# Optimization experiments

Measured on AMD Instinct MI355X. Metric: run time of the kernel, lower is better.

Reference implementation:

```python
import jax, jax.numpy as jnp
import numpy as np

N, E, L = 50000, 300000, 4
DN, DE, H, DO = 11, 3, 128, 2


def _ln(x, g, b, eps=1e-5):
    m = jnp.mean(x, axis=-1, keepdims=True)
    v = jnp.mean((x - m) ** 2, axis=-1, keepdims=True)
    return (x - m) * jax.lax.rsqrt(v + eps) * g + b


def _mlp(x, w1, b1, w2, b2, g, be):
    # Linear -> ReLU -> Linear -> LayerNorm (matches torch Sequential)
    h = jax.nn.relu(x @ w1 + b1)
    return _ln(h @ w2 + b2, g, be)


def setup_inputs() -> dict:
    key = jax.random.key(0)
    ks = iter(jax.random.split(key, 64))
    def nrm(shape, s=1.0):
        return jax.random.normal(next(ks), shape, jnp.float32) * s
    w = 0.02  # weight init scale
    inp = {
        'x': nrm((N, DN)),
        'edge_index': jax.random.randint(next(ks), (2, E), 0, N, jnp.int32),
        'edge_attr': nrm((E, DE)),
        'mean_vec_x': nrm((DN,)),
        'std_vec_x': jnp.ones((DN,), jnp.float32),
        'mean_vec_edge': nrm((DE,)),
        'std_vec_edge': jnp.ones((DE,), jnp.float32),
        # node encoder
        'ne_w1': nrm((DN, H), w), 'ne_b1': jnp.zeros((H,), jnp.float32),
        'ne_w2': nrm((H, H), w), 'ne_b2': jnp.zeros((H,), jnp.float32),
        'ne_g': jnp.ones((H,), jnp.float32), 'ne_be': jnp.zeros((H,), jnp.float32),
        # edge encoder
        'ee_w1': nrm((DE, H), w), 'ee_b1': jnp.zeros((H,), jnp.float32),
        'ee_w2': nrm((H, H), w), 'ee_b2': jnp.zeros((H,), jnp.float32),
        'ee_g': jnp.ones((H,), jnp.float32), 'ee_be': jnp.zeros((H,), jnp.float32),
        # processor edge MLPs (stacked over L layers): Linear(3H->H), Linear(H->H), LN
        'pe_w1': nrm((L, 3 * H, H), w), 'pe_b1': jnp.zeros((L, H), jnp.float32),
        'pe_w2': nrm((L, H, H), w), 'pe_b2': jnp.zeros((L, H), jnp.float32),
        'pe_g': jnp.ones((L, H), jnp.float32), 'pe_be': jnp.zeros((L, H), jnp.float32),
        # processor node MLPs: Linear(2H->H), Linear(H->H), LN
        'pn_w1': nrm((L, 2 * H, H), w), 'pn_b1': jnp.zeros((L, H), jnp.float32),
        'pn_w2': nrm((L, H, H), w), 'pn_b2': jnp.zeros((L, H), jnp.float32),
        'pn_g': jnp.ones((L, H), jnp.float32), 'pn_be': jnp.zeros((L, H), jnp.float32),
        # decoder: Linear(H->H) ReLU Linear(H->DO)
        'de_w1': nrm((H, H), w), 'de_b1': jnp.zeros((H,), jnp.float32),
        'de_w2': nrm((H, DO), w), 'de_b2': jnp.zeros((DO,), jnp.float32),
    }
    return inp


def reference(x, edge_index, edge_attr, mean_vec_x, std_vec_x, mean_vec_edge, std_vec_edge,
              ne_w1, ne_b1, ne_w2, ne_b2, ne_g, ne_be,
              ee_w1, ee_b1, ee_w2, ee_b2, ee_g, ee_be,
              pe_w1, pe_b1, pe_w2, pe_b2, pe_g, pe_be,
              pn_w1, pn_b1, pn_w2, pn_b2, pn_g, pn_be,
              de_w1, de_b1, de_w2, de_b2):
    x = (x - mean_vec_x) / std_vec_x
    e = (edge_attr - mean_vec_edge) / std_vec_edge
    x = _mlp(x, ne_w1, ne_b1, ne_w2, ne_b2, ne_g, ne_be)   # [N, H]
    e = _mlp(e, ee_w1, ee_b1, ee_w2, ee_b2, ee_g, ee_be)   # [E, H]
    row, col = edge_index[0], edge_index[1]
    for i in range(L):
        # edge update: gather endpoints, concat with edge feature, residual
        msg_in = jnp.concatenate([x[row], x[col], e], axis=-1)  # [E, 3H]
        e = e + _mlp(msg_in, pe_w1[i], pe_b1[i], pe_w2[i], pe_b2[i], pe_g[i], pe_be[i])
        # aggregate messages (= updated edge_attr) at target nodes (col), sum-aggr
        agg = jax.ops.segment_sum(e, col, num_segments=N)       # [N, H]
        node_in = jnp.concatenate([x, agg], axis=-1)             # [N, 2H]
        x = x + _mlp(node_in, pn_w1[i], pn_b1[i], pn_w2[i], pn_b2[i], pn_g[i], pn_be[i])
    return jax.nn.relu(x @ de_w1 + de_b1) @ de_w2 + de_b2       # [N, DO]
```

## Files before the change

### kernel.cpp

```cpp
#include <hip/hip_runtime.h>
#include <hip/hip_bf16.h>


#define NN 50000
#define EE 300000

typedef unsigned int u32;
typedef unsigned short u16;
typedef __attribute__((ext_vector_type(8))) short bf16x8;
typedef __attribute__((ext_vector_type(4))) float f32x4;

__device__ __forceinline__ float bf2f(u16 v){ return __uint_as_float(((u32)v) << 16); }
__device__ __forceinline__ u16 f2bf(float f){
  u32 u = __float_as_uint(f);
  return (u16)((u + 0x7fffu + ((u >> 16) & 1u)) >> 16);
}
#define MFMA __builtin_amdgcn_mfma_f32_16x16x32_bf16

struct CD { const void* src; float* dst; int n; };
struct IngestArgs { CD d[34]; };

__global__ __launch_bounds__(256)
void ingest_kernel(IngestArgs a, const u32* __restrict__ probe) {
  const bool isbf = (probe[0] == 0x3F803F80u);
  const CD c = a.d[blockIdx.y];
  for (int i = blockIdx.x*256 + threadIdx.x; i < c.n; i += gridDim.x*256) {
    c.dst[i] = isbf ? bf2f(((const u16*)c.src)[i]) : ((const float*)c.src)[i];
  }
}

struct PackDesc { const float* src; u16* dst; int K; int Ksrc; };
struct PackArgs { PackDesc d[20]; };

__global__ __launch_bounds__(256)
void pack_b_kernel(PackArgs pa) {
  const PackDesc p = pa.d[blockIdx.y];
  const int total = (p.K >> 5) * 512;
  for (int idx = blockIdx.x*256 + threadIdx.x; idx < total; idx += gridDim.x*256) {
    const int lane = idx & 63;
    const int tile = idx >> 6;
    const int nt = tile & 7, kt = tile >> 3;
    const int col = nt*16 + (lane & 15);
    const int k0  = kt*32 + (lane >> 4) * 8;
    u32 w4[4];
    #pragma unroll
    for (int jj = 0; jj < 4; ++jj) {
      const int ka = k0 + 2*jj, kb = k0 + 2*jj + 1;
      const u16 lo = (ka < p.Ksrc) ? f2bf(p.src[(size_t)ka * 128 + col]) : (u16)0;
      const u16 hi = (kb < p.Ksrc) ? f2bf(p.src[(size_t)kb * 128 + col]) : (u16)0;
      w4[jj] = (u32)lo | ((u32)hi << 16);
    }
    *(uint4*)(p.dst + (size_t)idx * 8) = make_uint4(w4[0], w4[1], w4[2], w4[3]);
  }
}

__global__ __launch_bounds__(256)
void zero_kernel(int4* __restrict__ p, int n4) {
  for (int i = blockIdx.x*256 + threadIdx.x; i < n4; i += gridDim.x*256)
    p[i] = make_int4(0, 0, 0, 0);
}

__global__ __launch_bounds__(256)
void hist_kernel(const int* __restrict__ ei, int* __restrict__ deg) {
  for (int i = blockIdx.x*256 + threadIdx.x; i < EE; i += gridDim.x*256)
    atomicAdd(&deg[ei[EE + i]], 1);
}

__global__ __launch_bounds__(1024)
void scan_kernel(const int* __restrict__ deg, int* __restrict__ start,
                 int* __restrict__ cursor) {
  __shared__ int sums[1024];
  const int t = threadIdx.x;
  const int base = t * 49;
  int s = 0;
  for (int j = 0; j < 49; ++j) { const int i = base + j; if (i < NN) s += deg[i]; }
  sums[t] = s; __syncthreads();
  for (int off = 1; off < 1024; off <<= 1) {
    int v = (t >= off) ? sums[t - off] : 0;
    __syncthreads();
    sums[t] += v;
    __syncthreads();
  }
  int ex = (t == 0) ? 0 : sums[t - 1];
  for (int j = 0; j < 49; ++j) {
    const int i = base + j;
    if (i < NN) { start[i] = ex; cursor[i] = ex; ex += deg[i]; }
  }
  if (t == 1023) start[NN] = ex;
}

__global__ __launch_bounds__(256)
void scatter_kernel(const int* __restrict__ ei, int* __restrict__ cursor,
                    int* __restrict__ perm, int* __restrict__ src_p,
                    int* __restrict__ dst_p) {
  for (int i = blockIdx.x*256 + threadIdx.x; i < EE; i += gridDim.x*256) {
    const int c = ei[EE + i];
    const int pos = atomicAdd(&cursor[c], 1);
    perm[pos]  = i;
    src_p[pos] = ei[i];
    dst_p[pos] = c;
  }
}

template<int KIN, int MODE>
__global__ __launch_bounds__(256)
void enc_mfma(const u16* __restrict__ w1pk, const float* __restrict__ b1,
              const u16* __restrict__ w2pk, const float* __restrict__ b2,
              const float* __restrict__ g,  const float* __restrict__ be,
              const float* __restrict__ raw, const float* __restrict__ mean,
              const float* __restrict__ stdv, const int* __restrict__ perm,
              float* __restrict__ x, u16* __restrict__ outb, int nrows)
{
  constexpr int STR = 296;
  __shared__ u16 As[64 * STR];
  const int lane  = threadIdx.x & 63;
  const int wv    = threadIdx.x >> 6;
  const int col_l = lane & 15;
  const int quad  = lane >> 4;
  const int m0    = wv * 16;
  const int r0    = blockIdx.x * 64;

  for (int t = lane; t < 256; t += 64)
    ((u32*)As)[(m0 + (t >> 4)) * 148 + (t & 15)] = 0u;
  for (int t = lane; t < 16 * KIN; t += 64) {
    const int r = t / KIN, k = t - r * KIN;
    int srow = min(r0 + m0 + r, nrows - 1);
    if constexpr (MODE == 1) srow = perm[srow];
    const float v = (raw[(size_t)srow * KIN + k] - mean[k]) / stdv[k];
    As[(m0 + r) * STR + k] = f2bf(v);
  }

  float b1v[8], b2v[8], gv[8], bev[8];
  #pragma unroll
  for (int nt = 0; nt < 8; ++nt) {
    b1v[nt] = b1[nt*16 + col_l]; b2v[nt] = b2[nt*16 + col_l];
    gv[nt]  = g [nt*16 + col_l]; bev[nt] = be[nt*16 + col_l];
  }

  const f32x4 zf = {0.f, 0.f, 0.f, 0.f};
  const bf16x8* bq1 = (const bf16x8*)w1pk;
  const bf16x8* bq2 = (const bf16x8*)w2pk;
  const u16* arow = As + (size_t)(m0 + col_l) * STR + quad * 8;

  f32x4 acc[8];
  #pragma unroll
  for (int nt = 0; nt < 8; ++nt) acc[nt] = zf;
  {
    const bf16x8 af = *(const bf16x8*)(arow);
    #pragma unroll
    for (int nt = 0; nt < 8; ++nt)
      acc[nt] = MFMA(af, bq1[nt*64 + lane], acc[nt], 0, 0, 0);
  }
  #pragma unroll
  for (int nt = 0; nt < 8; ++nt) {
    #pragma unroll
    for (int rg = 0; rg < 4; ++rg) {
      const float hv = fmaxf(acc[nt][rg] + b1v[nt], 0.f);
      As[(size_t)(m0 + quad*4 + rg) * STR + 32 + nt*16 + col_l] = f2bf(hv);
    }
  }
  f32x4 acc2[8];
  #pragma unroll
  for (int nt = 0; nt < 8; ++nt) acc2[nt] = zf;
  #pragma unroll
  for (int kt = 0; kt < 4; ++kt) {
    const bf16x8 af = *(const bf16x8*)(arow + 32 + kt * 32);
    #pragma unroll
    for (int nt = 0; nt < 8; ++nt)
      acc2[nt] = MFMA(af, bq2[(kt*8+nt)*64 + lane], acc2[nt], 0, 0, 0);
  }
  #pragma unroll
  for (int rg = 0; rg < 4; ++rg) {
    float v[8];
    float s1 = 0.f, s2 = 0.f;
    #pragma unroll
    for (int nt = 0; nt < 8; ++nt) {
      v[nt] = acc2[nt][rg] + b2v[nt];
      s1 += v[nt]; s2 += v[nt]*v[nt];
    }
    #pragma unroll
    for (int off = 1; off < 16; off <<= 1) {
      s1 += __shfl_xor(s1, off);
      s2 += __shfl_xor(s2, off);
    }
    const float mu   = s1 * (1.f/128.f);
    const float var  = s2 * (1.f/128.f) - mu*mu;
    const float rstd = rsqrtf(var + 1e-5f);
    const int rloc = m0 + quad*4 + rg;
    const int row  = r0 + rloc;
    #pragma unroll
    for (int nt = 0; nt < 8; ++nt) {
      const float y = (v[nt] - mu) * rstd * gv[nt] + bev[nt];
      As[(size_t)rloc * STR + 160 + nt*16 + col_l] = f2bf(y);
      if (MODE == 0 && row < nrows) x[(size_t)row*128 + nt*16 + col_l] = y;
    }
  }
  #pragma unroll
  for (int r = 0; r < 16; ++r) {
    const int row = r0 + m0 + r;
    if (row < nrows)
      ((u32*)(outb + (size_t)row * 128))[lane] =
          ((const u32*)(As + (size_t)(m0 + r) * STR + 160))[lane];
  }
}

__global__ __launch_bounds__(256, 1)
void edge_mfma(const u16* __restrict__ w1pk, const float* __restrict__ b1,
               const u16* __restrict__ w2pk, const float* __restrict__ b2,
               const float* __restrict__ g, const float* __restrict__ be,
               const u16* __restrict__ xb, u16* __restrict__ eb,
               const int* __restrict__ src_p, const int* __restrict__ dst_p)
{
  extern __shared__ u16 lds[];
  u16* lw1 = lds;
  u16* lh  = lds + 49152;

  const int lane = threadIdx.x & 63;
  const int wv   = threadIdx.x >> 6;
  const int m    = lane & 15;
  const int q    = lane >> 4;
  const int rbase = wv * 32;

  for (int i = threadIdx.x; i < 6144; i += 256)
    ((uint4*)lw1)[i] = ((const uint4*)w1pk)[i];

  bf16x8 w2r[32];
  #pragma unroll
  for (int f = 0; f < 32; ++f)
    w2r[f] = ((const bf16x8*)w2pk)[f*64 + lane];

  float b1v[8], b2v[8], gv[8], bev[8];
  #pragma unroll
  for (int nt = 0; nt < 8; ++nt) {
    b1v[nt] = b1[nt*16 + m]; b2v[nt] = b2[nt*16 + m];
    gv[nt]  = g [nt*16 + m]; bev[nt] = be[nt*16 + m];
  }
  __syncthreads();

  const int ntiles = (EE + 127) >> 7;
  bf16x8 A[2][12];

  auto loadA = [&](int t) {
    #pragma unroll
    for (int ms = 0; ms < 2; ++ms) {
      const int grow = min(t*128 + rbase + ms*16 + m, EE-1);
      const u16* p0 = xb + (size_t)src_p[grow] * 128 + q*8;
      const u16* p1 = xb + (size_t)dst_p[grow] * 128 + q*8;
      const u16* p2 = eb + (size_t)grow * 128 + q*8;
      #pragma unroll
      for (int kt = 0; kt < 4; ++kt) {
        A[ms][kt]   = *(const bf16x8*)(p0 + kt*32);
        A[ms][4+kt] = *(const bf16x8*)(p1 + kt*32);
        A[ms][8+kt] = *(const bf16x8*)(p2 + kt*32);
      }
    }
  };

  loadA(blockIdx.x);
  for (int t = blockIdx.x; t < ntiles; t += 256) {
    #pragma unroll
    for (int nt = 0; nt < 8; ++nt) {
      f32x4 c0 = {0.f,0.f,0.f,0.f}, c1 = {0.f,0.f,0.f,0.f};
      #pragma unroll
      for (int kt = 0; kt < 12; ++kt) {
        const bf16x8 bf = *(const bf16x8*)(lw1 + (size_t)(kt*8+nt)*512 + lane*8);
        c0 = MFMA(A[0][kt], bf, c0, 0, 0, 0);
        c1 = MFMA(A[1][kt], bf, c1, 0, 0, 0);
      }
      #pragma unroll
      for (int ms = 0; ms < 2; ++ms) {
        #pragma unroll
        for (int rg = 0; rg < 4; ++rg) {
          const float cc = (ms == 0) ? c0[rg] : c1[rg];
          const float hv = fmaxf(cc + b1v[nt], 0.f);
          const int row = rbase + ms*16 + q*4 + rg;
          const int col = nt*16 + m;
          lh[row*128 + ((((col>>3) ^ (row&7)))<<3) + (col&7)] = f2bf(hv);
        }
      }
    }
    const int tn = t + 256;
    if (tn < ntiles) loadA(tn);
    f32x4 acc2[2][8];
    #pragma unroll
    for (int ms = 0; ms < 2; ++ms)
      #pragma unroll
      for (int nt = 0; nt < 8; ++nt) acc2[ms][nt] = {0.f,0.f,0.f,0.f};
    #pragma unroll
    for (int kt2 = 0; kt2 < 4; ++kt2) {
      const int ra = rbase + m, rb = rbase + 16 + m;
      const bf16x8 h0 = *(const bf16x8*)(lh + ra*128 + (((kt2*4+q) ^ (ra&7))<<3));
      const bf16x8 h1 = *(const bf16x8*)(lh + rb*128 + (((kt2*4+q) ^ (rb&7))<<3));
      #pragma unroll
      for (int nt = 0; nt < 8; ++nt) {
        acc2[0][nt] = MFMA(h0, w2r[kt2*8+nt], acc2[0][nt], 0, 0, 0);
        acc2[1][nt] = MFMA(h1, w2r[kt2*8+nt], acc2[1][nt], 0, 0, 0);
      }
    }
    #pragma unroll
    for (int ms = 0; ms < 2; ++ms) {
      #pragma unroll
      for (int rg = 0; rg < 4; ++rg) {
        const int grow  = t*128 + rbase + ms*16 + q*4 + rg;
        const int growc = min(grow, EE-1);
        float eo[8];
        #pragma unroll
        for (int nt = 0; nt < 8; ++nt)
          eo[nt] = bf2f(eb[(size_t)growc*128 + nt*16 + m]);
        float v[8]; float s1 = 0.f, s2 = 0.f;
        #pragma unroll
        for (int nt = 0; nt < 8; ++nt) {
          v[nt] = acc2[ms][nt][rg] + b2v[nt];
          s1 += v[nt]; s2 += v[nt]*v[nt];
        }
        #pragma unroll
        for (int off = 1; off < 16; off <<= 1) {
          s1 += __shfl_xor(s1, off);
          s2 += __shfl_xor(s2, off);
        }
        const float mu   = s1 * (1.f/128.f);
        const float rstd = rsqrtf(s2*(1.f/128.f) - mu*mu + 1e-5f);
        if (grow < EE) {
          #pragma unroll
          for (int nt = 0; nt < 8; ++nt) {
            const float y = (v[nt] - mu) * rstd * gv[nt] + bev[nt];
            eb[(size_t)grow*128 + nt*16 + m] = f2bf(y + eo[nt]);
          }
        }
      }
    }
  }
}

__global__ __launch_bounds__(256, 1)
void node_mfma(const u16* __restrict__ w1pk, const float* __restrict__ b1,
               const u16* __restrict__ w2pk, const float* __restrict__ b2,
               const float* __restrict__ g, const float* __restrict__ be,
               float* __restrict__ x, u16* __restrict__ xb,
               const u16* __restrict__ eb, const int* __restrict__ start)
{
  extern __shared__ u16 lds[];
  u16* lw1 = lds;
  u16* lh  = lds + 32768;
  u16* lag = lds + 49152;

  const int lane = threadIdx.x & 63;
  const int wv   = threadIdx.x >> 6;
  const int m    = lane & 15;
  const int q    = lane >> 4;
  const int rbase = wv * 32;

  for (int i = threadIdx.x; i < 4096; i += 256)
    ((uint4*)lw1)[i] = ((const uint4*)w1pk)[i];

  bf16x8 w2r[32];
  #pragma unroll
  for (int f = 0; f < 32; ++f)
    w2r[f] = ((const bf16x8*)w2pk)[f*64 + lane];

  float b1v[8], b2v[8], gv[8], bev[8];
  #pragma unroll
  for (int nt = 0; nt < 8; ++nt) {
    b1v[nt] = b1[nt*16 + m]; b2v[nt] = b2[nt*16 + m];
    gv[nt]  = g [nt*16 + m]; bev[nt] = be[nt*16 + m];
  }
  __syncthreads();

  const int ntiles = (NN + 127) >> 7;
  for (int t = blockIdx.x; t < ntiles; t += 256) {
    const int gbase = t*128 + rbase;
    const int sa = start[min(gbase + (lane & 31), NN)];
    const int sb = start[min(gbase + (lane & 31) + 1, NN)];
    for (int r = 0; r < 32; ++r) {
      const int s0 = __shfl(sa, r), s1 = __shfl(sb, r);
      float a0 = 0.f, a1 = 0.f;
      int j = s0;
      for (; j + 4 <= s1; j += 4) {
        const u32 q0 = ((const u32*)(eb + (size_t)(j  ) * 128))[lane];
        const u32 q1 = ((const u32*)(eb + (size_t)(j+1) * 128))[lane];
        const u32 q2 = ((const u32*)(eb + (size_t)(j+2) * 128))[lane];
        const u32 q3 = ((const u32*)(eb + (size_t)(j+3) * 128))[lane];
        a0 += bf2f((u16)q0) + bf2f((u16)q1) + bf2f((u16)q2) + bf2f((u16)q3);
        a1 += bf2f((u16)(q0>>16)) + bf2f((u16)(q1>>16)) + bf2f((u16)(q2>>16)) + bf2f((u16)(q3>>16));
      }
      for (; j < s1; ++j) {
        const u32 qq = ((const u32*)(eb + (size_t)j * 128))[lane];
        a0 += bf2f((u16)qq); a1 += bf2f((u16)(qq>>16));
      }
      const int lr = rbase + r;
      const int ch = (lane >> 2) ^ (lr & 7);
      *(u32*)(lag + lr*128 + (ch<<3) + ((2*lane) & 7)) =
          (u32)f2bf(a0) | ((u32)f2bf(a1) << 16);
    }
    bf16x8 A[2][8];
    #pragma unroll
    for (int ms = 0; ms < 2; ++ms) {
      const int grow = min(gbase + ms*16 + m, NN-1);
      const u16* p0 = xb + (size_t)grow * 128 + q*8;
      const int lr = rbase + ms*16 + m;
      #pragma unroll
      for (int kt = 0; kt < 4; ++kt) {
        A[ms][kt]   = *(const bf16x8*)(p0 + kt*32);
        A[ms][4+kt] = *(const bf16x8*)(lag + lr*128 + (((kt*4+q) ^ (lr&7))<<3));
      }
    }
    #pragma unroll
    for (int nt = 0; nt < 8; ++nt) {
      f32x4 c0 = {0.f,0.f,0.f,0.f}, c1 = {0.f,0.f,0.f,0.f};
      #pragma unroll
      for (int kt = 0; kt < 8; ++kt) {
        const bf16x8 bf = *(const bf16x8*)(lw1 + (size_t)(kt*8+nt)*512 + lane*8);
        c0 = MFMA(A[0][kt], bf, c0, 0, 0, 0);
        c1 = MFMA(A[1][kt], bf, c1, 0, 0, 0);
      }
      #pragma unroll
      for (int ms = 0; ms < 2; ++ms) {
        #pragma unroll
        for (int rg = 0; rg < 4; ++rg) {
          const float cc = (ms == 0) ? c0[rg] : c1[rg];
          const float hv = fmaxf(cc + b1v[nt], 0.f);
          const int row = rbase + ms*16 + q*4 + rg;
          const int col = nt*16 + m;
          lh[row*128 + ((((col>>3) ^ (row&7)))<<3) + (col&7)] = f2bf(hv);
        }
      }
    }
    f32x4 acc2[2][8];
    #pragma unroll
    for (int ms = 0; ms < 2; ++ms)
      #pragma unroll
      for (int nt = 0; nt < 8; ++nt) acc2[ms][nt] = {0.f,0.f,0.f,0.f};
    #pragma unroll
    for (int kt2 = 0; kt2 < 4; ++kt2) {
      const int ra = rbase + m, rb = rbase + 16 + m;
      const bf16x8 h0 = *(const bf16x8*)(lh + ra*128 + (((kt2*4+q) ^ (ra&7))<<3));
      const bf16x8 h1 = *(const bf16x8*)(lh + rb*128 + (((kt2*4+q) ^ (rb&7))<<3));
      #pragma unroll
      for (int nt = 0; nt < 8; ++nt) {
        acc2[0][nt] = MFMA(h0, w2r[kt2*8+nt], acc2[0][nt], 0, 0, 0);
        acc2[1][nt] = MFMA(h1, w2r[kt2*8+nt], acc2[1][nt], 0, 0, 0);
      }
    }
    #pragma unroll
    for (int ms = 0; ms < 2; ++ms) {
      #pragma unroll
      for (int rg = 0; rg < 4; ++rg) {
        const int grow  = t*128 + rbase + ms*16 + q*4 + rg;
        const int growc = min(grow, NN-1);
        float xo[8];
        #pragma unroll
        for (int nt = 0; nt < 8; ++nt)
          xo[nt] = x[(size_t)growc*128 + nt*16 + m];
        float v[8]; float s1 = 0.f, s2 = 0.f;
        #pragma unroll
        for (int nt = 0; nt < 8; ++nt) {
          v[nt] = acc2[ms][nt][rg] + b2v[nt];
          s1 += v[nt]; s2 += v[nt]*v[nt];
        }
        #pragma unroll
        for (int off = 1; off < 16; off <<= 1) {
          s1 += __shfl_xor(s1, off);
          s2 += __shfl_xor(s2, off);
        }
        const float mu   = s1 * (1.f/128.f);
        const float rstd = rsqrtf(s2*(1.f/128.f) - mu*mu + 1e-5f);
        if (grow < NN) {
          #pragma unroll
          for (int nt = 0; nt < 8; ++nt) {
            const float y  = (v[nt] - mu) * rstd * gv[nt] + bev[nt];
            const float xn = y + xo[nt];
            x [(size_t)grow*128 + nt*16 + m] = xn;
            xb[(size_t)grow*128 + nt*16 + m] = f2bf(xn);
          }
        }
      }
    }
  }
}

constexpr int TM  = 8;
constexpr int WPB = 2;

__global__ __launch_bounds__(WPB*64)
void decoder_kernel(const float* __restrict__ x,
                    const float* __restrict__ w1, const float* __restrict__ b1,
                    const float* __restrict__ w2, const float* __restrict__ b2,
                    void* __restrict__ out, const u32* __restrict__ probe,
                    int nrows)
{
  const bool isbf = (probe[0] == 0x3F803F80u);
  const int lane = threadIdx.x & 63;
  const int wv   = threadIdx.x >> 6;
  const int wgl  = blockIdx.x * WPB + wv;
  const int nw   = gridDim.x * WPB;
  extern __shared__ float smem[];
  float* in_s = smem + wv * (TM * 128);

  const float2* w1p = ((const float2*)w1) + lane;
  const float b1l = b1[2*lane], b1h = b1[2*lane+1];
  const float2 wA = ((const float2*)w2)[2*lane];
  const float2 wB = ((const float2*)w2)[2*lane+1];
  const float c0 = b2[0], c1 = b2[1];

  for (int r0 = wgl * TM; r0 < nrows; r0 += nw * TM) {
    const int rcnt = min(TM, nrows - r0);
    for (int t = lane; t < rcnt * 128; t += 64) {
      const int r = t >> 7, k = t & 127;
      in_s[r*128 + k] = x[(size_t)(r0+r)*128 + k];
    }
    float a0[TM], a1[TM];
    #pragma unroll
    for (int r=0;r<TM;++r){ a0[r]=0.f; a1[r]=0.f; }
    for (int k = 0; k < 128; k += 2) {
      const float2 wa = w1p[(k  )*64];
      const float2 wb = w1p[(k+1)*64];
      #pragma unroll
      for (int r=0;r<TM;++r){
        const float2 av = *(const float2*)(in_s + r*128 + k);
        a0[r] = fmaf(av.x, wa.x, a0[r]); a1[r] = fmaf(av.x, wa.y, a1[r]);
        a0[r] = fmaf(av.y, wb.x, a0[r]); a1[r] = fmaf(av.y, wb.y, a1[r]);
      }
    }
    for (int r = 0; r < rcnt; ++r) {
      const float h0 = fmaxf(a0[r] + b1l, 0.f);
      const float h1 = fmaxf(a1[r] + b1h, 0.f);
      float p0 = fmaf(h0, wA.x, h1 * wB.x);
      float p1 = fmaf(h0, wA.y, h1 * wB.y);
      #pragma unroll
      for (int off = 32; off; off >>= 1) {
        p0 += __shfl_xor(p0, off);
        p1 += __shfl_xor(p1, off);
      }
      if (lane == 0) {
        const float o0 = p0 + c0;
        const float o1 = p1 + c1;
        if (isbf) ((u32*)out)[r0 + r] = (u32)f2bf(o0) | ((u32)f2bf(o1) << 16);
        else      *(float2*)((float*)out + (size_t)(r0 + r)*2) = make_float2(o0, o1);
      }
    }
  }
}

extern "C" void kernel_launch(void* const* d_in, const int* in_sizes, int n_in,
                              void* d_out, int out_size, void* d_ws, size_t ws_size,
                              hipStream_t stream) {
  static const int src_idx[34] = {0,2,3,4,5,6,
    7,8,9,10,11,12, 13,14,15,16,17,18,
    19,20,21,22,23,24, 25,26,27,28,29,30, 31,32,33,34};
  static const int sz[34] = {550000,900000,11,11,3,3,
    1408,128,16384,128,128,128,
    384,128,16384,128,128,128,
    196608,512,65536,512,512,512,
    131072,512,65536,512,512,512,
    16384,128,256,2};

  IngestArgs ia;
  const float* cp[35] = {};
  float* w = (float*)d_ws;
  for (int j = 0; j < 34; ++j) {
    ia.d[j].src = d_in[src_idx[j]];
    ia.d[j].dst = w;
    ia.d[j].n   = sz[j];
    cp[src_idx[j]] = w;
    w += sz[j];
  }
  w = (float*)(((uintptr_t)w + 63) & ~(uintptr_t)63);
  float* x   = w;
  u16*   xb  = (u16*)(x + (size_t)NN*128);
  u16*   e   = xb + (size_t)NN*128;
  u16*   pk  = e  + (size_t)EE*128;
  u16* pk_pe1 = pk;
  u16* pk_pe2 = pk_pe1 + (size_t)4*384*128;
  u16* pk_pn1 = pk_pe2 + (size_t)4*128*128;
  u16* pk_pn2 = pk_pn1 + (size_t)4*256*128;
  u16* pk_ne1 = pk_pn2 + (size_t)4*128*128;
  u16* pk_ne2 = pk_ne1 + (size_t)32*128;
  u16* pk_ee1 = pk_ne2 + (size_t)128*128;
  u16* pk_ee2 = pk_ee1 + (size_t)32*128;
  int* deg    = (int*)(pk_ee2 + (size_t)128*128);
  int* start  = deg + NN;
  int* cursor = start + NN + 1;
  int* perm   = cursor + NN;
  int* src_p  = perm + EE;
  int* dst_p  = src_p + EE;

  const u32* probe = (const u32*)d_in[4];
  const int* ei    = (const int*)d_in[1];

  hipFuncSetAttribute((const void*)edge_mfma,
                      hipFuncAttributeMaxDynamicSharedMemorySize, 131072);
  hipFuncSetAttribute((const void*)node_mfma,
                      hipFuncAttributeMaxDynamicSharedMemorySize, 131072);

  ingest_kernel<<<dim3(128, 34), 256, 0, stream>>>(ia, probe);

  PackArgs pa;
  for (int l = 0; l < 4; ++l) {
    pa.d[l*4+0] = { cp[19] + (size_t)l*384*128, pk_pe1 + (size_t)l*384*128, 384, 384 };
    pa.d[l*4+1] = { cp[21] + (size_t)l*128*128, pk_pe2 + (size_t)l*128*128, 128, 128 };
    pa.d[l*4+2] = { cp[25] + (size_t)l*256*128, pk_pn1 + (size_t)l*256*128, 256, 256 };
    pa.d[l*4+3] = { cp[27] + (size_t)l*128*128, pk_pn2 + (size_t)l*128*128, 128, 128 };
  }
  pa.d[16] = { cp[7],  pk_ne1,  32,  11 };
  pa.d[17] = { cp[9],  pk_ne2, 128, 128 };
  pa.d[18] = { cp[13], pk_ee1,  32,   3 };
  pa.d[19] = { cp[15], pk_ee2, 128, 128 };
  pack_b_kernel<<<dim3(24, 20), 256, 0, stream>>>(pa);

  zero_kernel<<<dim3(64), 256, 0, stream>>>((int4*)deg, NN/4);
  hist_kernel<<<dim3(512), 256, 0, stream>>>(ei, deg);
  scan_kernel<<<dim3(1), 1024, 0, stream>>>(deg, start, cursor);
  scatter_kernel<<<dim3(512), 256, 0, stream>>>(ei, cursor, perm, src_p, dst_p);

  enc_mfma<11, 0><<<dim3((NN + 63)/64), 256, 0, stream>>>(
      pk_ne1, cp[8], pk_ne2, cp[10], cp[11], cp[12],
      cp[0], cp[3], cp[4], nullptr, x, xb, NN);
  enc_mfma<3, 1><<<dim3((EE + 63)/64), 256, 0, stream>>>(
      pk_ee1, cp[14], pk_ee2, cp[16], cp[17], cp[18],
      cp[2], cp[5], cp[6], perm, nullptr, e, EE);

  for (int l = 0; l < 4; ++l) {
    edge_mfma<<<dim3(256), 256, 131072, stream>>>(
        pk_pe1 + (size_t)l*384*128, cp[20] + l*128,
        pk_pe2 + (size_t)l*128*128, cp[22] + l*128,
        cp[23] + l*128, cp[24] + l*128,
        xb, e, src_p, dst_p);
    node_mfma<<<dim3(256), 256, 131072, stream>>>(
        pk_pn1 + (size_t)l*256*128, cp[26] + l*128,
        pk_pn2 + (size_t)l*128*128, cp[28] + l*128,
        cp[29] + l*128, cp[30] + l*128,
        x, xb, e, start);
  }

  decoder_kernel<<<dim3((NN + TM*WPB - 1)/(TM*WPB)), dim3(WPB*64),
                   (size_t)(WPB*TM*128*4), stream>>>(
      x, cp[31], cp[32], cp[33], cp[34], d_out, probe, NN);
}
```

Measured before the change: 1.304 ms.

## Use 512-thread blocks with 16 rows per wave in edge/node MFMA kernels

The edge and node MLP kernels go from 256 to 512 threads per block, and each wave now handles 16 rows instead of 32. This halves per-wave accumulator and A-fragment registers so more waves can hide gather latency. Bias, gamma and beta are read from global memory when needed instead of being held in registers. Outputs are staged through LDS and written back as coalesced row stores instead of strided scattered bf16 stores. The cost is that LDS-staged weights are re-read per 16-row tile, giving less MFMA reuse per B fragment. The launch_bounds(512,2) setting with 131072 bytes of dynamic LDS may not actually allow two blocks per CU.

```diff
diff --git a/kernel.cpp b/kernel.cpp
--- a/kernel.cpp
+++ b/kernel.cpp
@@ -204,7 +204,7 @@
   }
 }
 
-__global__ __launch_bounds__(256, 1)
+__global__ __launch_bounds__(512, 2)
 void edge_mfma(const u16* __restrict__ w1pk, const float* __restrict__ b1,
                const u16* __restrict__ w2pk, const float* __restrict__ b2,
                const float* __restrict__ g, const float* __restrict__ be,
@@ -219,40 +219,30 @@
   const int wv   = threadIdx.x >> 6;
   const int m    = lane & 15;
   const int q    = lane >> 4;
-  const int rbase = wv * 32;
-
-  for (int i = threadIdx.x; i < 6144; i += 256)
+  const int rbase = wv * 16;
+
+  for (int i = threadIdx.x; i < 6144; i += 512)
     ((uint4*)lw1)[i] = ((const uint4*)w1pk)[i];
 
   bf16x8 w2r[32];
   #pragma unroll
   for (int f = 0; f < 32; ++f)
     w2r[f] = ((const bf16x8*)w2pk)[f*64 + lane];
-
-  float b1v[8], b2v[8], gv[8], bev[8];
-  #pragma unroll
-  for (int nt = 0; nt < 8; ++nt) {
-    b1v[nt] = b1[nt*16 + m]; b2v[nt] = b2[nt*16 + m];
-    gv[nt]  = g [nt*16 + m]; bev[nt] = be[nt*16 + m];
-  }
   __syncthreads();
 
   const int ntiles = (EE + 127) >> 7;
-  bf16x8 A[2][12];
+  bf16x8 A[12];
 
   auto loadA = [&](int t) {
-    #pragma unroll
-    for (int ms = 0; ms < 2; ++ms) {
-      const int grow = min(t*128 + rbase + ms*16 + m, EE-1);
-      const u16* p0 = xb + (size_t)src_p[grow] * 128 + q*8;
-      const u16* p1 = xb + (size_t)dst_p[grow] * 128 + q*8;
-      const u16* p2 = eb + (size_t)grow * 128 + q*8;
-      #pragma unroll
-      for (int kt = 0; kt < 4; ++kt) {
-        A[ms][kt]   = *(const bf16x8*)(p0 + kt*32);
-        A[ms][4+kt] = *(const bf16x8*)(p1 + kt*32);
-        A[ms][8+kt] = *(const bf16x8*)(p2 + kt*32);
-      }
+    const int grow = min(t*128 + rbase + m, EE-1);
+    const u16* p0 = xb + (size_t)src_p[grow] * 128 + q*8;
+    const u16* p1 = xb + (size_t)dst_p[grow] * 128 + q*8;
+    const u16* p2 = eb + (size_t)grow * 128 + q*8;
+    #pragma unroll
+    for (int kt = 0; kt < 4; ++kt) {
+      A[kt]   = *(const bf16x8*)(p0 + kt*32);
+      A[4+kt] = *(const bf16x8*)(p1 + kt*32);
+      A[8+kt] = *(const bf16x8*)(p2 + kt*32);
     }
   };
 
@@ -260,79 +250,73 @@
   for (int t = blockIdx.x; t < ntiles; t += 256) {
     #pragma unroll
     for (int nt = 0; nt < 8; ++nt) {
-      f32x4 c0 = {0.f,0.f,0.f,0.f}, c1 = {0.f,0.f,0.f,0.f};
+      f32x4 c = {0.f,0.f,0.f,0.f};
       #pragma unroll
       for (int kt = 0; kt < 12; ++kt) {
         const bf16x8 bf = *(const bf16x8*)(lw1 + (size_t)(kt*8+nt)*512 + lane*8);
-        c0 = MFMA(A[0][kt], bf, c0, 0, 0, 0);
-        c1 = MFMA(A[1][kt], bf, c1, 0, 0, 0);
-      }
-      #pragma unroll
-      for (int ms = 0; ms < 2; ++ms) {
-        #pragma unroll
-        for (int rg = 0; rg < 4; ++rg) {
-          const float cc = (ms == 0) ? c0[rg] : c1[rg];
-          const float hv = fmaxf(cc + b1v[nt], 0.f);
-          const int row = rbase + ms*16 + q*4 + rg;
-          const int col = nt*16 + m;
-          lh[row*128 + ((((col>>3) ^ (row&7)))<<3) + (col&7)] = f2bf(hv);
-        }
+        c = MFMA(A[kt], bf, c, 0, 0, 0);
+      }
+      const float b1n = b1[nt*16 + m];
+      #pragma unroll
+      for (int rg = 0; rg < 4; ++rg) {
+        const float hv = fmaxf(c[rg] + b1n, 0.f);
+        const int row = rbase + q*4 + rg;
+        const int col = nt*16 + m;
+        lh[row*128 + (((col>>3) ^ (row&7))<<3) + (col&7)] = f2bf(hv);
       }
     }
     const int tn = t + 256;
     if (tn < ntiles) loadA(tn);
-    f32x4 acc2[2][8];
-    #pragma unroll
-    for (int ms = 0; ms < 2; ++ms)
-      #pragma unroll
-      for (int nt = 0; nt < 8; ++nt) acc2[ms][nt] = {0.f,0.f,0.f,0.f};
+    f32x4 acc2[8];
+    #pragma unroll
+    for (int nt = 0; nt < 8; ++nt) acc2[nt] = {0.f,0.f,0.f,0.f};
     #pragma unroll
     for (int kt2 = 0; kt2 < 4; ++kt2) {
-      const int ra = rbase + m, rb = rbase + 16 + m;
+      const int ra = rbase + m;
       const bf16x8 h0 = *(const bf16x8*)(lh + ra*128 + (((kt2*4+q) ^ (ra&7))<<3));
-      const bf16x8 h1 = *(const bf16x8*)(lh + rb*128 + (((kt2*4+q) ^ (rb&7))<<3));
+      #pragma unroll
+      for (int nt = 0; nt < 8; ++nt)
+        acc2[nt] = MFMA(h0, w2r[kt2*8+nt], acc2[nt], 0, 0, 0);
+    }
+    #pragma unroll
+    for (int rg = 0; rg < 4; ++rg) {
+      const int rloc = q*4 + rg;
+      const int grow = min(t*128 + rbase + rloc, EE-1);
+      float v[8]; float s1 = 0.f, s2 = 0.f;
       #pragma unroll
       for (int nt = 0; nt < 8; ++nt) {
-        acc2[0][nt] = MFMA(h0, w2r[kt2*8+nt], acc2[0][nt], 0, 0, 0);
-        acc2[1][nt] = MFMA(h1, w2r[kt2*8+nt], acc2[1][nt], 0, 0, 0);
-      }
-    }
-    #pragma unroll
-    for (int ms = 0; ms < 2; ++ms) {
-      #pragma unroll
-      for (int rg = 0; rg < 4; ++rg) {
-        const int grow  = t*128 + rbase + ms*16 + q*4 + rg;
-        const int growc = min(grow, EE-1);
-        float eo[8];
-        #pragma unroll
-        for (int nt = 0; nt < 8; ++nt)
-          eo[nt] = bf2f(eb[(size_t)growc*128 + nt*16 + m]);
-        float v[8]; float s1 = 0.f, s2 = 0.f;
-        #pragma unroll
-        for (int nt = 0; nt < 8; ++nt) {
-          v[nt] = acc2[ms][nt][rg] + b2v[nt];
-          s1 += v[nt]; s2 += v[nt]*v[nt];
-        }
-        #pragma unroll
-        for (int off = 1; off < 16; off <<= 1) {
-          s1 += __shfl_xor(s1, off);
-          s2 += __shfl_xor(s2, off);
-        }
-        const float mu   = s1 * (1.f/128.f);
-        const float rstd = rsqrtf(s2*(1.f/128.f) - mu*mu + 1e-5f);
-        if (grow < EE) {
-          #pragma unroll
-          for (int nt = 0; nt < 8; ++nt) {
-            const float y = (v[nt] - mu) * rstd * gv[nt] + bev[nt];
-            eb[(size_t)grow*128 + nt*16 + m] = f2bf(y + eo[nt]);
-          }
-        }
-      }
-    }
-  }
-}
-
-__global__ __launch_bounds__(256, 1)
+        v[nt] = acc2[nt][rg] + b2[nt*16 + m];
+        s1 += v[nt]; s2 += v[nt]*v[nt];
+      }
+      #pragma unroll
+      for (int off = 1; off < 16; off <<= 1) {
+        s1 += __shfl_xor(s1, off);
+        s2 += __shfl_xor(s2, off);
+      }
+      const float mu   = s1 * (1.f/128.f);
+      const float rstd = rsqrtf(s2*(1.f/128.f) - mu*mu + 1e-5f);
+      #pragma unroll
+      for (int nt = 0; nt < 8; ++nt) {
+        const float y  = (v[nt] - mu) * rstd * g[nt*16 + m] + be[nt*16 + m];
+        const float eo = bf2f(eb[(size_t)grow*128 + nt*16 + m]);
+        const int row = rbase + rloc;
+        const int col = nt*16 + m;
+        lh[row*128 + (((col>>3) ^ (row&7))<<3) + (col&7)] = f2bf(y + eo);
+      }
+    }
+    #pragma unroll
+    for (int r = 0; r < 16; ++r) {
+      const int grow = t*128 + rbase + r;
+      if (grow < EE) {
+        const int ch = (lane >> 2) ^ (r & 7);
+        ((u32*)(eb + (size_t)grow * 128))[lane] =
+            *(const u32*)(lh + (rbase + r)*128 + (ch<<3) + 2*(lane & 3));
+      }
+    }
+  }
+}
+
+__global__ __launch_bounds__(512, 2)
 void node_mfma(const u16* __restrict__ w1pk, const float* __restrict__ b1,
                const u16* __restrict__ w2pk, const float* __restrict__ b2,
                const float* __restrict__ g, const float* __restrict__ be,
@@ -348,31 +332,23 @@
   const int wv   = threadIdx.x >> 6;
   const int m    = lane & 15;
   const int q    = lane >> 4;
-  const int rbase = wv * 32;
-
-  for (int i = threadIdx.x; i < 4096; i += 256)
+  const int rbase = wv * 16;
+
+  for (int i = threadIdx.x; i < 4096; i += 512)
     ((uint4*)lw1)[i] = ((const uint4*)w1pk)[i];
 
   bf16x8 w2r[32];
   #pragma unroll
   for (int f = 0; f < 32; ++f)
     w2r[f] = ((const bf16x8*)w2pk)[f*64 + lane];
-
-  float b1v[8], b2v[8], gv[8], bev[8];
-  #pragma unroll
-  for (int nt = 0; nt < 8; ++nt) {
-    b1v[nt] = b1[nt*16 + m]; b2v[nt] = b2[nt*16 + m];
-    gv[nt]  = g [nt*16 + m]; bev[nt] = be[nt*16 + m];
-  }
   __syncthreads();
 
   const int ntiles = (NN + 127) >> 7;
   for (int t = blockIdx.x; t < ntiles; t += 256) {
     const int gbase = t*128 + rbase;
-    const int sa = start[min(gbase + (lane & 31), NN)];
-    const int sb = start[min(gbase + (lane & 31) + 1, NN)];
-    for (int r = 0; r < 32; ++r) {
-      const int s0 = __shfl(sa, r), s1 = __shfl(sb, r);
+    const int sv = start[min(gbase + (lane & 31), NN)];
+    for (int r = 0; r < 16; ++r) {
+      const int s0 = __shfl(sv, r), s1 = __shfl(sv, r + 1);
       float a0 = 0.f, a1 = 0.f;
       int j = s0;
       for (; j + 4 <= s1; j += 4) {
@@ -388,91 +364,84 @@
         a0 += bf2f((u16)qq); a1 += bf2f((u16)(qq>>16));
       }
       const int lr = rbase + r;
-      const int ch = (lane >> 2) ^ (lr & 7);
-      *(u32*)(lag + lr*128 + (ch<<3) + ((2*lane) & 7)) =
+      const int ch = (lane >> 2) ^ (r & 7);
+      *(u32*)(lag + lr*128 + (ch<<3) + 2*(lane & 3)) =
           (u32)f2bf(a0) | ((u32)f2bf(a1) << 16);
     }
-    bf16x8 A[2][8];
-    #pragma unroll
-    for (int ms = 0; ms < 2; ++ms) {
-      const int grow = min(gbase + ms*16 + m, NN-1);
+    bf16x8 A[8];
+    {
+      const int grow = min(gbase + m, NN-1);
       const u16* p0 = xb + (size_t)grow * 128 + q*8;
-      const int lr = rbase + ms*16 + m;
+      const int lr = rbase + m;
       #pragma unroll
       for (int kt = 0; kt < 4; ++kt) {
-        A[ms][kt]   = *(const bf16x8*)(p0 + kt*32);
-        A[ms][4+kt] = *(const bf16x8*)(lag + lr*128 + (((kt*4+q) ^ (lr&7))<<3));
+        A[kt]   = *(const bf16x8*)(p0 + kt*32);
+        A[4+kt] = *(const bf16x8*)(lag + lr*128 + (((kt*4+q) ^ (m&7))<<3));
       }
     }
     #pragma unroll
     for (int nt = 0; nt < 8; ++nt) {
-      f32x4 c0 = {0.f,0.f,0.f,0.f}, c1 = {0.f,0.f,0.f,0.f};
+      f32x4 c = {0.f,0.f,0.f,0.f};
       #pragma unroll
       for (int kt = 0; kt < 8; ++kt) {
         const bf16x8 bf = *(const bf16x8*)(lw1 + (size_t)(kt*8+nt)*512 + lane*8);
-        c0 = MFMA(A[0][kt], bf, c0, 0, 0, 0);
-        c1 = MFMA(A[1][kt], bf, c1, 0, 0, 0);
-      }
-      #pragma unroll
-      for (int ms = 0; ms < 2; ++ms) {
-        #pragma unroll
-        for (int rg = 0; rg < 4; ++rg) {
-          const float cc = (ms == 0) ? c0[rg] : c1[rg];
-          const float hv = fmaxf(cc + b1v[nt], 0.f);
-          const int row = rbase + ms*16 + q*4 + rg;
-          const int col = nt*16 + m;
-          lh[row*128 + ((((col>>3) ^ (row&7)))<<3) + (col&7)] = f2bf(hv);
-        }
-      }
-    }
-    f32x4 acc2[2][8];
-    #pragma unroll
-    for (int ms = 0; ms < 2; ++ms)
-      #pragma unroll
-      for (int nt = 0; nt < 8; ++nt) acc2[ms][nt] = {0.f,0.f,0.f,0.f};
+        c = MFMA(A[kt], bf, c, 0, 0, 0);
+      }
+      const float b1n = b1[nt*16 + m];
+      #pragma unroll
+      for (int rg = 0; rg < 4; ++rg) {
+        const float hv = fmaxf(c[rg] + b1n, 0.f);
+        const int row = rbase + q*4 + rg;
+        const int col = nt*16 + m;
+        lh[row*128 + (((col>>3) ^ (row&7))<<3) + (col&7)] = f2bf(hv);
+      }
+    }
+    f32x4 acc2[8];
+    #pragma unroll
+    for (int nt = 0; nt < 8; ++nt) acc2[nt] = {0.f,0.f,0.f,0.f};
     #pragma unroll
     for (int kt2 = 0; kt2 < 4; ++kt2) {
-      const int ra = rbase + m, rb = rbase + 16 + m;
+      const int ra = rbase + m;
       const bf16x8 h0 = *(const bf16x8*)(lh + ra*128 + (((kt2*4+q) ^ (ra&7))<<3));
-      const bf16x8 h1 = *(const bf16x8*)(lh + rb*128 + (((kt2*4+q) ^ (rb&7))<<3));
+      #pragma unroll
+      for (int nt = 0; nt < 8; ++nt)
+        acc2[nt] = MFMA(h0, w2r[kt2*8+nt], acc2[nt], 0, 0, 0);
+    }
+    #pragma unroll
+    for (int rg = 0; rg < 4; ++rg) {
+      const int rloc = q*4 + rg;
+      const int grow = t*128 + rbase + rloc;
+      const int growc = min(grow, NN-1);
+      float v[8]; float s1 = 0.f, s2 = 0.f;
       #pragma unroll
       for (int nt = 0; nt < 8; ++nt) {
-        acc2[0][nt] = MFMA(h0, w2r[kt2*8+nt], acc2[0][nt], 0, 0, 0);
-        acc2[1][nt] = MFMA(h1, w2r[kt2*8+nt], acc2[1][nt], 0, 0, 0);
-      }
-    }
-    #pragma unroll
-    for (int ms = 0; ms < 2; ++ms) {
-      #pragma unroll
-      for (int rg = 0; rg < 4; ++rg) {
-        const int grow  = t*128 + rbase + ms*16 + q*4 + rg;
-        const int growc = min(grow, NN-1);
-        float xo[8];
-        #pragma unroll
-        for (int nt = 0; nt < 8; ++nt)
-          xo[nt] = x[(size_t)growc*128 + nt*16 + m];
-        float v[8]; float s1 = 0.f, s2 = 0.f;
-        #pragma unroll
-        for (int nt = 0; nt < 8; ++nt) {
-          v[nt] = acc2[ms][nt][rg] + b2v[nt];
-          s1 += v[nt]; s2 += v[nt]*v[nt];
-        }
-        #pragma unroll
-        for (int off = 1; off < 16; off <<= 1) {
-          s1 += __shfl_xor(s1, off);
-          s2 += __shfl_xor(s2, off);
-        }
-        const float mu   = s1 * (1.f/128.f);
-        const float rstd = rsqrtf(s2*(1.f/128.f) - mu*mu + 1e-5f);
-        if (grow < NN) {
-          #pragma unroll
-          for (int nt = 0; nt < 8; ++nt) {
-            const float y  = (v[nt] - mu) * rstd * gv[nt] + bev[nt];
-            const float xn = y + xo[nt];
-            x [(size_t)grow*128 + nt*16 + m] = xn;
-            xb[(size_t)grow*128 + nt*16 + m] = f2bf(xn);
-          }
-        }
+        v[nt] = acc2[nt][rg] + b2[nt*16 + m];
+        s1 += v[nt]; s2 += v[nt]*v[nt];
+      }
+      #pragma unroll
+      for (int off = 1; off < 16; off <<= 1) {
+        s1 += __shfl_xor(s1, off);
+        s2 += __shfl_xor(s2, off);
+      }
+      const float mu   = s1 * (1.f/128.f);
+      const float rstd = rsqrtf(s2*(1.f/128.f) - mu*mu + 1e-5f);
+      #pragma unroll
+      for (int nt = 0; nt < 8; ++nt) {
+        const float y  = (v[nt] - mu) * rstd * g[nt*16 + m] + be[nt*16 + m];
+        const float xn = y + x[(size_t)growc*128 + nt*16 + m];
+        if (grow < NN) x[(size_t)grow*128 + nt*16 + m] = xn;
+        const int row = rbase + rloc;
+        const int col = nt*16 + m;
+        lh[row*128 + (((col>>3) ^ (row&7))<<3) + (col&7)] = f2bf(xn);
+      }
+    }
+    #pragma unroll
+    for (int r = 0; r < 16; ++r) {
+      const int grow = t*128 + rbase + r;
+      if (grow < NN) {
+        const int ch = (lane >> 2) ^ (r & 7);
+        ((u32*)(xb + (size_t)grow * 128))[lane] =
+            *(const u32*)(lh + (rbase + r)*128 + (ch<<3) + 2*(lane & 3));
       }
     }
   }
@@ -620,12 +589,12 @@
       cp[2], cp[5], cp[6], perm, nullptr, e, EE);
 
   for (int l = 0; l < 4; ++l) {
-    edge_mfma<<<dim3(256), 256, 131072, stream>>>(
+    edge_mfma<<<dim3(256), dim3(512), 131072, stream>>>(
         pk_pe1 + (size_t)l*384*128, cp[20] + l*128,
         pk_pe2 + (size_t)l*128*128, cp[22] + l*128,
         cp[23] + l*128, cp[24] + l*128,
         xb, e, src_p, dst_p);
-    node_mfma<<<dim3(256), 256, 131072, stream>>>(
+    node_mfma<<<dim3(256), dim3(512), 131072, stream>>>(
         pk_pn1 + (size_t)l*256*128, cp[26] + l*128,
         pk_pn2 + (size_t)l*128*128, cp[28] + l*128,
         cp[29] + l*128, cp[30] + l*128,
```

Measured after the change: 2.045 ms. 56.9% more time.
